# Kernel tuning notes

Hardware: AMD Instinct MI355X
Metric: run time of the kernel (lower is better)

## Reference

```python
import jax, jax.numpy as jnp
import numpy as np

E = 768      # embed_dim
H = 12       # num_heads
D = E // H   # head_dim = 64
G = 8        # num_groups (grouped 1x1 conv)
MAX_S = 197  # max_seq_len
RED = 8      # SE reduction ratio
S, B = 197, 64


def grouped_linear(x, w, b):
    """Grouped 1x1 conv as grouped linear. x: [..., Cin], w: [Cout, Cin//G], b: [Cout]."""
    cout = w.shape[0]
    cin = x.shape[-1]
    xg = x.reshape(x.shape[:-1] + (G, cin // G))
    wg = w.reshape(G, cout // G, cin // G)
    y = jnp.einsum('...gi,goi->...go', xg, wg)
    return y.reshape(x.shape[:-1] + (cout,)) + b


def channel_shuffle(x):
    """Shuffle channels (last dim) across G groups, matching torch channel_shuffle."""
    c = x.shape[-1]
    xg = x.reshape(x.shape[:-1] + (G, c // G))
    return jnp.swapaxes(xg, -1, -2).reshape(x.shape)


def layernorm(x, g, b, eps=1e-5):
    mu = jnp.mean(x, axis=-1, keepdims=True)
    var = jnp.var(x, axis=-1, keepdims=True)
    return (x - mu) * jax.lax.rsqrt(var + eps) * g + b


def setup_inputs() -> dict:
    rng = jax.random.key(0)
    ks = jax.random.split(rng, 16)
    std = 0.02
    return {
        'query': jax.random.normal(ks[0], (S, B, E), jnp.float32),
        'key':   jax.random.normal(ks[1], (S, B, E), jnp.float32),
        'value': jax.random.normal(ks[2], (S, B, E), jnp.float32),
        'qkv_w': jax.random.normal(ks[3], (3 * E, E // G), jnp.float32) * std,
        'qkv_b': jnp.zeros((3 * E,), jnp.float32),
        'out_w': jax.random.normal(ks[4], (E, E // G), jnp.float32) * std,
        'out_b': jnp.zeros((E,), jnp.float32),
        'rel_pos': jax.random.normal(ks[5], (2 * MAX_S - 1, D), jnp.float32) * std,
        'ln_g': jnp.ones((E,), jnp.float32),
        'ln_b': jnp.zeros((E,), jnp.float32),
        'fc1_w': jax.random.normal(ks[6], (E, E // RED), jnp.float32) * std,
        'fc1_b': jnp.zeros((E // RED,), jnp.float32),
        'fc2_w': jax.random.normal(ks[7], (E // RED, E), jnp.float32) * std,
        'fc2_b': jnp.zeros((E,), jnp.float32),
    }


def reference(query, key, value, qkv_w, qkv_b, out_w, out_b, rel_pos,
              ln_g, ln_b, fc1_w, fc1_b, fc2_w, fc2_b):
    seq_len, bsz, embed_dim = query.shape
    scaling = float(D) ** -0.5

    x = jnp.transpose(query, (1, 0, 2))              # [B, S, E]
    qkv = grouped_linear(x, qkv_w, qkv_b)            # [B, S, 3E]
    qkv = channel_shuffle(qkv)                       # [B, S, 3E]
    q, k, v = jnp.split(qkv, 3, axis=-1)             # each [B, S, E]

    def heads(t):                                    # [B, S, E] -> [B, H, S, D]
        return jnp.transpose(t.reshape(bsz, seq_len, H, D), (0, 2, 1, 3))
    q, k, v = heads(q) * scaling, heads(k), heads(v)

    attn_w = jnp.einsum('bhsd,bhtd->bhst', q, k)     # content-content

    # decoupled relative-position attention (note: slice, not skew, per source)
    rel = rel_pos[MAX_S - seq_len: MAX_S + seq_len - 1]           # [2S-1, D]
    content_pos = jnp.einsum('bhsd,rd->bhsr', q, rel)[..., seq_len - 1: 2 * seq_len - 1]
    pos_content = jnp.einsum('rd,bhtd->bhrt', rel, k)[:, :, seq_len - 1: 2 * seq_len - 1, :]
    attn_w = attn_w + content_pos + pos_content

    probs = jax.nn.softmax(attn_w, axis=-1)          # [B, H, S, S]
    attn = jnp.einsum('bhst,bhtd->bhsd', probs, v)   # [B, H, S, D]
    attn = jnp.transpose(attn, (0, 2, 1, 3)).reshape(bsz, seq_len, E)  # [B, S, E]

    # squeeze-excite style feature calibration gating
    scale = jax.nn.sigmoid(
        jnp.dot(jax.nn.gelu(jnp.dot(layernorm(attn, ln_g, ln_b), fc1_w) + fc1_b), fc2_w) + fc2_b)
    attn = attn * scale

    out = grouped_linear(attn, out_w, out_b)         # [B, S, E]
    out = jnp.transpose(out, (1, 0, 2))              # [S, B, E]

    avg_weights = jnp.sum(probs, axis=1) / H         # [B, S, S]
    return out, avg_weights
```

## Files before the change

kernel.cpp:

```cpp
#include <hip/hip_runtime.h>
#include <hip/hip_bf16.h>

constexpr int S = 197;
constexpr int B = 64;
constexpr int E = 768;
constexpr int H = 12;
constexpr int D = 64;
constexpr int M = S * B;
constexpr size_t SBE = (size_t)M * E;
constexpr int PST = 208;

typedef short bf16x8 __attribute__((ext_vector_type(8)));
typedef float f32x4 __attribute__((ext_vector_type(4)));
typedef unsigned int u32x4 __attribute__((ext_vector_type(4)));

__device__ __forceinline__ unsigned short f2b(float x) {
  unsigned int u = __float_as_uint(x);
  return (unsigned short)((u + 0x7FFFu + ((u >> 16) & 1u)) >> 16);
}
__device__ __forceinline__ float b2f(unsigned short u) {
  return __uint_as_float((unsigned int)u << 16);
}

__global__ __launch_bounds__(256) void mha_wprep(const float* __restrict__ w1,
                                                 const float* __restrict__ w2,
                                                 const float* __restrict__ lng,
                                                 const float* __restrict__ lnb,
                                                 const float* __restrict__ b1,
                                                 const float* __restrict__ rel,
                                                 unsigned short* __restrict__ w1t,
                                                 unsigned short* __restrict__ w2t,
                                                 float* __restrict__ cgb,
                                                 float* __restrict__ cbb,
                                                 unsigned short* __restrict__ relb) {
  const int bid = blockIdx.x, tid = threadIdx.x;
  if (bid < 288) {
    int idx = bid * 256 + tid;
    int n = idx / 768, k = idx - n * 768;
    w1t[idx] = f2b(lng[k] * w1[(size_t)k * 96 + n]);
  } else if (bid < 576) {
    int idx = (bid - 288) * 256 + tid;
    int n = idx / 96, k = idx - n * 96;
    w2t[idx] = f2b(w2[(size_t)k * 768 + n]);
  } else if (bid == 576) {
    if (tid < 96) {
      float cg = 0.f, cb = 0.f;
      for (int k = 0; k < 768; ++k) {
        float wv = w1[(size_t)k * 96 + tid];
        cg += lng[k] * wv;
        cb += lnb[k] * wv;
      }
      cgb[tid] = cg;
      cbb[tid] = cb + b1[tid];
    }
  } else {
    int idx = (bid - 577) * 256 + tid;
    int s2 = idx >> 6, d = idx & 63;
    float v = (s2 < S) ? rel[(size_t)(S - 1 + s2) * D + d] : 0.f;
    relb[idx] = f2b(v);
  }
}

__global__ __launch_bounds__(256) void mha_qkv_gemm(const float* __restrict__ x,
                                                    const float* __restrict__ w,
                                                    const float* __restrict__ bias,
                                                    unsigned short* __restrict__ y) {
  __shared__ __align__(16) unsigned short Xs[64 * 104];
  __shared__ __align__(16) unsigned short Wsl[96 * 104];
  __shared__ float bias_s[96];
  const int m0 = blockIdx.x * 64;
  const int n0 = blockIdx.y * 96;
  const int g = blockIdx.y / 3;
  const int tid = threadIdx.x;

  for (int i = tid; i < 64 * 24; i += 256) {
    int r = i / 24, c4 = i - r * 24;
    float4 v = *reinterpret_cast<const float4*>(
        &x[(size_t)(m0 + r) * E + g * 96 + c4 * 4]);
    unsigned short* dst = Xs + r * 104 + c4 * 4;
    dst[0] = f2b(v.x); dst[1] = f2b(v.y); dst[2] = f2b(v.z); dst[3] = f2b(v.w);
  }
  for (int i = tid; i < 96 * 24; i += 256) {
    int n = i / 24, c4 = i - n * 24;
    float4 v = *reinterpret_cast<const float4*>(&w[(size_t)(n0 + n) * 96 + c4 * 4]);
    unsigned short* dst = Wsl + n * 104 + c4 * 4;
    dst[0] = f2b(v.x); dst[1] = f2b(v.y); dst[2] = f2b(v.z); dst[3] = f2b(v.w);
  }
  if (tid < 96) bias_s[tid] = bias[n0 + tid];
  __syncthreads();

  const int lane = tid & 63, wv = tid >> 6;
  const int l15 = lane & 15, l4 = lane >> 4;

  const unsigned short* xrow = Xs + (16 * wv + l15) * 104 + l4 * 8;
  bf16x8 a0 = *(const bf16x8*)(xrow);
  bf16x8 a1 = *(const bf16x8*)(xrow + 32);
  bf16x8 a2 = *(const bf16x8*)(xrow + 64);

  f32x4 acc[6];
#pragma unroll
  for (int nf = 0; nf < 6; ++nf) acc[nf] = (f32x4){0.f, 0.f, 0.f, 0.f};
#pragma unroll
  for (int nf = 0; nf < 6; ++nf) {
    const unsigned short* wrow = Wsl + (nf * 16 + l15) * 104 + l4 * 8;
    f32x4 a = acc[nf];
    a = __builtin_amdgcn_mfma_f32_16x16x32_bf16(a0, *(const bf16x8*)(wrow), a, 0, 0, 0);
    a = __builtin_amdgcn_mfma_f32_16x16x32_bf16(a1, *(const bf16x8*)(wrow + 32), a, 0, 0, 0);
    a = __builtin_amdgcn_mfma_f32_16x16x32_bf16(a2, *(const bf16x8*)(wrow + 64), a, 0, 0, 0);
    acc[nf] = a;
  }

  const int mloc = m0 + 16 * wv + 4 * l4;
#pragma unroll
  for (int nf = 0; nf < 6; ++nf) {
    int p = nf * 16 + l15;
    float bv = bias_s[p];
#pragma unroll
    for (int r = 0; r < 4; ++r)
      y[(size_t)(mloc + r) * 2304 + n0 + p] = f2b(acc[nf][r] + bv);
  }
}

__global__ __launch_bounds__(256) void mha_qkv_shuffle(const unsigned short* __restrict__ y,
                                                       const float* __restrict__ rel,
                                                       unsigned short* __restrict__ qb,
                                                       unsigned short* __restrict__ kb,
                                                       unsigned short* __restrict__ vb) {
  const int tid = threadIdx.x;
  const int lane = tid & 63;
  const int g = lane >> 3, j = lane & 7;
  const int d = j * 8 + g;
  const int wrow = tid >> 6;
  const int rbase = blockIdx.x * 16;

  float relv[4];
  int sA[4], bA[4];
#pragma unroll
  for (int r8 = 0; r8 < 4; ++r8) {
    int rowl = rbase + r8 * 4 + wrow;
    sA[r8] = rowl >> 6;
    bA[r8] = rowl & 63;
    relv[r8] = rel[(size_t)(S - 1 + sA[r8]) * D + d];
  }

  for (int h = 0; h < H; ++h) {
#pragma unroll
    for (int r8 = 0; r8 < 4; ++r8) {
      int rowl = rbase + r8 * 4 + wrow;
      const unsigned short* yr = y + (size_t)rowl * 2304 + g * 288 + h * 8 + j;
      size_t o = (((size_t)bA[r8] * H + h) * S + sA[r8]) * D + d;
      float vq = b2f(yr[0]);
      float vk = b2f(yr[96]);
      float vv = b2f(yr[192]);
      qb[o] = f2b(0.125f * vq + relv[r8]);
      kb[o] = f2b(vk + relv[r8]);
      vb[o] = f2b(vv);
    }
  }
}

__global__ __launch_bounds__(256) void mha_fattn(
    const unsigned short* __restrict__ qb, const unsigned short* __restrict__ kb,
    const unsigned short* __restrict__ vb, const unsigned short* __restrict__ relb,
    float* __restrict__ context, unsigned short* __restrict__ probs, int bh0) {
  __shared__ __align__(16) unsigned short KtPt[64 * 136];
  __shared__ __align__(16) unsigned short Vh[64 * 136];
  unsigned short* Kt = KtPt;
  unsigned short* Pt = KtPt;

  const int id = blockIdx.x;
  const int xcd = id & 7;
  const int rr = id >> 3;
  const int stile = rr & 3;
  const int bhl = xcd + 8 * (rr >> 2);
  const int bh = bh0 + bhl;
  const int b_ = bh / H, h_ = bh - b_ * H;
  const int s0 = stile * 64;
  const int tid = threadIdx.x;
  const int lane = tid & 63, w = tid >> 6;
  const int l15 = lane & 15, l4 = lane >> 4;
  const int vt = tid & 63;
  const int vdb = (tid >> 6) * 8;

  const unsigned short* qg = qb + (((size_t)bh * S + (s0 + 16 * w + l15)) << 6) + l4 * 8;
  const unsigned short* rg = relb + (((size_t)(s0 + 16 * w + l15)) << 6) + l4 * 8;
  bf16x8 aq0 = *(const bf16x8*)(qg);
  bf16x8 aq1 = *(const bf16x8*)(qg + 32);
  bf16x8 aq2 = *(const bf16x8*)(rg);
  bf16x8 aq3 = *(const bf16x8*)(rg + 32);

  auto loadK = [&](int tc, u32x4* kv, u32x4* rv) {
#pragma unroll
    for (int ii = 0; ii < 2; ++ii) {
      int idx = tid + ii * 256;
      int r = idx >> 3, c = idx & 7;
      int tg = tc * 64 + r;
      kv[ii] = (u32x4){0, 0, 0, 0};
      rv[ii] = (u32x4){0, 0, 0, 0};
      if (tg < S) {
        kv[ii] = *(const u32x4*)(kb + (((size_t)bh * S + tg) << 6) + c * 8);
        u32x4 rvv = *(const u32x4*)(relb + ((size_t)tg << 6) + c * 8);
        rv[ii] = rvv ^ 0x80008000u;
      }
    }
  };

  f32x4 acc[13];
#pragma unroll
  for (int i = 0; i < 13; ++i) acc[i] = (f32x4){0.f, 0.f, 0.f, 0.f};

  u32x4 kvA[2], rvA[2], kvB[2], rvB[2];
  loadK(0, kvA, rvA);

#pragma unroll
  for (int tc = 0; tc < 4; ++tc) {
    u32x4* kvc = (tc & 1) ? kvB : kvA;
    u32x4* rvc = (tc & 1) ? rvB : rvA;
#pragma unroll
    for (int ii = 0; ii < 2; ++ii) {
      int idx = tid + ii * 256;
      int r = idx >> 3, c = idx & 7;
      *(u32x4*)(Kt + r * 136 + c * 8) = kvc[ii];
      *(u32x4*)(Kt + r * 136 + 64 + c * 8) = rvc[ii];
    }
    if (tc < 3) loadK(tc + 1, (tc & 1) ? kvA : kvB, (tc & 1) ? rvA : rvB);
    __syncthreads();
#pragma unroll
    for (int tf = 0; tf < 4; ++tf) {
      if (tc == 3 && tf > 0) continue;
      const unsigned short* kbse = Kt + (tf * 16 + l15) * 136 + l4 * 8;
      f32x4 a = acc[tc * 4 + tf];
      a = __builtin_amdgcn_mfma_f32_16x16x32_bf16(aq0, *(const bf16x8*)(kbse), a, 0, 0, 0);
      a = __builtin_amdgcn_mfma_f32_16x16x32_bf16(aq1, *(const bf16x8*)(kbse + 32), a, 0, 0, 0);
      a = __builtin_amdgcn_mfma_f32_16x16x32_bf16(aq2, *(const bf16x8*)(kbse + 64), a, 0, 0, 0);
      a = __builtin_amdgcn_mfma_f32_16x16x32_bf16(aq3, *(const bf16x8*)(kbse + 96), a, 0, 0, 0);
      acc[tc * 4 + tf] = a;
    }
    __syncthreads();
  }

  u32x4 v1[4];
#pragma unroll
  for (int ii = 0; ii < 4; ++ii) {
    int t = (ii & 1) * 64 + vt;
    int d0 = vdb + (ii >> 1) * 32;
    v1[ii] = *(const u32x4*)(vb + (((size_t)bh * S + t) << 6) + d0);
  }

  if (l15 >= 5) acc[12] = (f32x4){-3.0e38f, -3.0e38f, -3.0e38f, -3.0e38f};
  float inv[4];
#pragma unroll
  for (int r = 0; r < 4; ++r) {
    float m = acc[0][r];
#pragma unroll
    for (int tf = 1; tf < 13; ++tf) m = fmaxf(m, acc[tf][r]);
#pragma unroll
    for (int off = 1; off < 16; off <<= 1) m = fmaxf(m, __shfl_xor(m, off, 64));
    float s = 0.f;
#pragma unroll
    for (int tf = 0; tf < 13; ++tf) {
      float e = __expf(acc[tf][r] - m);
      acc[tf][r] = e;
      s += e;
    }
#pragma unroll
    for (int off = 1; off < 16; off <<= 1) s += __shfl_xor(s, off, 64);
    inv[r] = 1.f / s;
  }

  f32x4 ov[4];
#pragma unroll
  for (int df = 0; df < 4; ++df) ov[df] = (f32x4){0.f, 0.f, 0.f, 0.f};

#pragma unroll
  for (int tf = 0; tf < 8; ++tf)
#pragma unroll
    for (int r = 0; r < 4; ++r)
      Pt[(16 * w + 4 * l4 + r) * 136 + tf * 16 + l15] = f2b(acc[tf][r] * inv[r]);
#pragma unroll
  for (int ii = 0; ii < 4; ++ii) {
    int t = (ii & 1) * 64 + vt;
    int d0 = vdb + (ii >> 1) * 32;
    const unsigned short* vp = (const unsigned short*)&v1[ii];
#pragma unroll
    for (int j = 0; j < 8; ++j) Vh[(d0 + j) * 136 + t] = vp[j];
  }
  __syncthreads();

  u32x4 v2[4];
#pragma unroll
  for (int ii = 0; ii < 4; ++ii) {
    int t = 128 + (ii & 1) * 64 + vt;
    int d0 = vdb + (ii >> 1) * 32;
    v2[ii] = (u32x4){0, 0, 0, 0};
    if (t < S) v2[ii] = *(const u32x4*)(vb + (((size_t)bh * S + t) << 6) + d0);
  }

  {
    const int r2 = tid >> 2;
    const int sg = s0 + r2;
    if (sg < S) {
#pragma unroll
      for (int j = 0; j < 4; ++j) {
        int c = (tid & 3) + 4 * j;
        u32x4 pv = *(const u32x4*)(Pt + r2 * 136 + c * 8);
        *(u32x4*)(probs + ((size_t)bhl * S + sg) * PST + c * 8) = pv;
      }
    }
  }
  {
    bf16x8 ap[4];
#pragma unroll
    for (int kf = 0; kf < 4; ++kf)
      ap[kf] = *(const bf16x8*)(Pt + (16 * w + l15) * 136 + kf * 32 + l4 * 8);
#pragma unroll
    for (int df = 0; df < 4; ++df) {
      const unsigned short* vbse = Vh + (df * 16 + l15) * 136 + l4 * 8;
      f32x4 o = ov[df];
#pragma unroll
      for (int kf = 0; kf < 4; ++kf)
        o = __builtin_amdgcn_mfma_f32_16x16x32_bf16(ap[kf], *(const bf16x8*)(vbse + kf * 32), o, 0, 0, 0);
      ov[df] = o;
    }
  }
  __syncthreads();

#pragma unroll
  for (int tf = 8; tf < 13; ++tf)
#pragma unroll
    for (int r = 0; r < 4; ++r)
      Pt[(16 * w + 4 * l4 + r) * 136 + (tf - 8) * 16 + l15] = f2b(acc[tf][r] * inv[r]);
#pragma unroll
  for (int r = 0; r < 4; ++r)
    Pt[(16 * w + 4 * l4 + r) * 136 + 80 + l15] = 0;
#pragma unroll
  for (int ii = 0; ii < 4; ++ii) {
    int t0h = (ii & 1) * 64 + vt;
    int d0 = vdb + (ii >> 1) * 32;
    if (t0h < 96) {
      const unsigned short* vp = (const unsigned short*)&v2[ii];
#pragma unroll
      for (int j = 0; j < 8; ++j) Vh[(d0 + j) * 136 + t0h] = vp[j];
    }
  }
  __syncthreads();

  {
    const int r2 = tid >> 2;
    const int sg = s0 + r2;
    if (sg < S) {
#pragma unroll
      for (int j = 0; j < 3; ++j) {
        int c = (tid & 3) + 4 * j;
        if (c < 10) {
          u32x4 pv = *(const u32x4*)(Pt + r2 * 136 + c * 8);
          *(u32x4*)(probs + ((size_t)bhl * S + sg) * PST + 128 + c * 8) = pv;
        }
      }
    }
  }
  {
    bf16x8 ap[3];
#pragma unroll
    for (int kf = 0; kf < 3; ++kf)
      ap[kf] = *(const bf16x8*)(Pt + (16 * w + l15) * 136 + kf * 32 + l4 * 8);
#pragma unroll
    for (int df = 0; df < 4; ++df) {
      const unsigned short* vbse = Vh + (df * 16 + l15) * 136 + l4 * 8;
      f32x4 o = ov[df];
#pragma unroll
      for (int kf = 0; kf < 3; ++kf)
        o = __builtin_amdgcn_mfma_f32_16x16x32_bf16(ap[kf], *(const bf16x8*)(vbse + kf * 32), o, 0, 0, 0);
      ov[df] = o;
    }
  }

#pragma unroll
  for (int df = 0; df < 4; ++df)
#pragma unroll
    for (int r = 0; r < 4; ++r) {
      int sg = s0 + 16 * w + 4 * l4 + r;
      if (sg < S)
        context[((size_t)b_ * S + sg) * E + h_ * 64 + df * 16 + l15] = ov[df][r];
    }
}

__global__ __launch_bounds__(256) void mha_avgred(const unsigned short* __restrict__ probs,
                                                  float* __restrict__ avg, int b0) {
  const int bs = blockIdx.x;
  const int bl = bs / S, s = bs - bl * S;
  const int t = threadIdx.x;
  if (t >= S) return;
  float acc = 0.f;
#pragma unroll
  for (int h = 0; h < H; ++h)
    acc += b2f(probs[(((size_t)bl * H + h) * S + s) * PST + t]);
  avg[(((size_t)(b0 + bl)) * S + s) * S + t] = acc * (1.f / H);
}

__global__ __launch_bounds__(128) void mha_fc1ln(const float* __restrict__ ctx,
                                                 const unsigned short* __restrict__ w1t,
                                                 const float* __restrict__ cgb,
                                                 const float* __restrict__ cbb,
                                                 unsigned short* __restrict__ h1) {
  __shared__ __align__(16) unsigned short As[32 * 104];
  __shared__ __align__(16) unsigned short Wl[48 * 104];
  __shared__ float smu[32], sinv[32];
  const int m0 = blockIdx.x * 32;
  const int n0 = blockIdx.y * 48;
  const int tid = threadIdx.x;
  const int lane = tid & 63, w = tid >> 6;
  const int l15 = lane & 15, l4 = lane >> 4;
  const int r = tid >> 2, q = tid & 3;

  float s1 = 0.f, s2 = 0.f;
  f32x4 acc[3];
#pragma unroll
  for (int nf = 0; nf < 3; ++nf) acc[nf] = (f32x4){0.f, 0.f, 0.f, 0.f};

  for (int c = 0; c < 8; ++c) {
    const int k0 = c * 96;
    {
      const float* xr = ctx + (size_t)(m0 + r) * E + k0 + q * 24;
      unsigned short* ar = As + r * 104 + q * 24;
#pragma unroll
      for (int j = 0; j < 6; ++j) {
        float4 v = *reinterpret_cast<const float4*>(xr + j * 4);
        s1 += v.x + v.y + v.z + v.w;
        s2 += v.x * v.x + v.y * v.y + v.z * v.z + v.w * v.w;
        ar[j * 4 + 0] = f2b(v.x); ar[j * 4 + 1] = f2b(v.y);
        ar[j * 4 + 2] = f2b(v.z); ar[j * 4 + 3] = f2b(v.w);
      }
    }
    for (int i = tid; i < 48 * 12; i += 128) {
      int n = i / 12, c8 = i - n * 12;
      *(u32x4*)(Wl + n * 104 + c8 * 8) =
          *(const u32x4*)(w1t + (size_t)(n0 + n) * E + k0 + c8 * 8);
    }
    __syncthreads();
    const unsigned short* arow = As + (16 * w + l15) * 104 + l4 * 8;
    bf16x8 a0 = *(const bf16x8*)(arow);
    bf16x8 a1 = *(const bf16x8*)(arow + 32);
    bf16x8 a2 = *(const bf16x8*)(arow + 64);
#pragma unroll
    for (int nf = 0; nf < 3; ++nf) {
      const unsigned short* wr = Wl + (nf * 16 + l15) * 104 + l4 * 8;
      f32x4 a = acc[nf];
      a = __builtin_amdgcn_mfma_f32_16x16x32_bf16(a0, *(const bf16x8*)(wr), a, 0, 0, 0);
      a = __builtin_amdgcn_mfma_f32_16x16x32_bf16(a1, *(const bf16x8*)(wr + 32), a, 0, 0, 0);
      a = __builtin_amdgcn_mfma_f32_16x16x32_bf16(a2, *(const bf16x8*)(wr + 64), a, 0, 0, 0);
      acc[nf] = a;
    }
    __syncthreads();
  }

  s1 += __shfl_xor(s1, 1, 64); s1 += __shfl_xor(s1, 2, 64);
  s2 += __shfl_xor(s2, 1, 64); s2 += __shfl_xor(s2, 2, 64);
  if (q == 0) {
    float mu = s1 * (1.f / E);
    float var = s2 * (1.f / E) - mu * mu;
    smu[r] = mu;
    sinv[r] = rsqrtf(var + 1e-5f);
  }
  __syncthreads();

#pragma unroll
  for (int nf = 0; nf < 3; ++nf) {
    int n = n0 + nf * 16 + l15;
    float cg = cgb[n], cb = cbb[n];
#pragma unroll
    for (int rr = 0; rr < 4; ++rr) {
      int ml = 16 * w + 4 * l4 + rr;
      float u = sinv[ml] * (acc[nf][rr] - smu[ml] * cg) + cb;
      float gl = 0.5f * u * (1.f + tanhf(0.7978845608028654f * (u + 0.044715f * u * u * u)));
      h1[(size_t)(m0 + ml) * 96 + n] = f2b(gl);
    }
  }
}

__global__ __launch_bounds__(256) void mha_fc2(const unsigned short* __restrict__ h1,
                                               const unsigned short* __restrict__ w2t,
                                               const float* __restrict__ bias,
                                               const float* __restrict__ ctx,
                                               unsigned short* __restrict__ attn2) {
  __shared__ __align__(16) unsigned short Hs[64 * 104];
  __shared__ __align__(16) unsigned short Wl[192 * 104];
  const int m0 = blockIdx.x * 64;
  const int n0 = blockIdx.y * 192;
  const int tid = threadIdx.x;
  const int lane = tid & 63, w = tid >> 6;
  const int l15 = lane & 15, l4 = lane >> 4;

  for (int i = tid; i < 64 * 12; i += 256) {
    int rr = i / 12, c8 = i - rr * 12;
    *(u32x4*)(Hs + rr * 104 + c8 * 8) =
        *(const u32x4*)(h1 + (size_t)(m0 + rr) * 96 + c8 * 8);
  }
  for (int i = tid; i < 192 * 12; i += 256) {
    int n = i / 12, c8 = i - n * 12;
    *(u32x4*)(Wl + n * 104 + c8 * 8) =
        *(const u32x4*)(w2t + (size_t)(n0 + n) * 96 + c8 * 8);
  }
  __syncthreads();

  const unsigned short* arow = Hs + (16 * w + l15) * 104 + l4 * 8;
  bf16x8 a0 = *(const bf16x8*)(arow);
  bf16x8 a1 = *(const bf16x8*)(arow + 32);
  bf16x8 a2 = *(const bf16x8*)(arow + 64);

#pragma unroll
  for (int nf = 0; nf < 12; ++nf) {
    const unsigned short* wr = Wl + (nf * 16 + l15) * 104 + l4 * 8;
    f32x4 a = (f32x4){0.f, 0.f, 0.f, 0.f};
    a = __builtin_amdgcn_mfma_f32_16x16x32_bf16(a0, *(const bf16x8*)(wr), a, 0, 0, 0);
    a = __builtin_amdgcn_mfma_f32_16x16x32_bf16(a1, *(const bf16x8*)(wr + 32), a, 0, 0, 0);
    a = __builtin_amdgcn_mfma_f32_16x16x32_bf16(a2, *(const bf16x8*)(wr + 64), a, 0, 0, 0);
    int n = n0 + nf * 16 + l15;
    float bv = bias[n];
#pragma unroll
    for (int rr = 0; rr < 4; ++rr) {
      int m = m0 + 16 * w + 4 * l4 + rr;
      float val = a[rr] + bv;
      float sg = 1.f / (1.f + __expf(-val));
      float cv = ctx[(size_t)m * E + n];
      attn2[(size_t)m * E + n] = f2b(cv * sg);
    }
  }
}

__global__ __launch_bounds__(256) void mha_out(const unsigned short* __restrict__ attn2,
                                               const float* __restrict__ w,
                                               const float* __restrict__ bias,
                                               float* __restrict__ outp) {
  __shared__ __align__(16) unsigned short Asl[64 * 104];
  __shared__ __align__(16) unsigned short Wl[96 * 104];
  __shared__ float bias_s[96];
  const int m0 = blockIdx.x * 64;
  const int g = blockIdx.y;
  const int n0 = g * 96;
  const int tid = threadIdx.x;
  const int lane = tid & 63, w_ = tid >> 6;
  const int l15 = lane & 15, l4 = lane >> 4;

  for (int i = tid; i < 64 * 12; i += 256) {
    int rr = i / 12, c8 = i - rr * 12;
    *(u32x4*)(Asl + rr * 104 + c8 * 8) =
        *(const u32x4*)(attn2 + (size_t)(m0 + rr) * E + n0 + c8 * 8);
  }
  for (int i = tid; i < 96 * 24; i += 256) {
    int n = i / 24, c4 = i - n * 24;
    float4 v = *reinterpret_cast<const float4*>(&w[(size_t)(n0 + n) * 96 + c4 * 4]);
    unsigned short* dst = Wl + n * 104 + c4 * 4;
    dst[0] = f2b(v.x); dst[1] = f2b(v.y); dst[2] = f2b(v.z); dst[3] = f2b(v.w);
  }
  if (tid < 96) bias_s[tid] = bias[n0 + tid];
  __syncthreads();

  const unsigned short* arow = Asl + (16 * w_ + l15) * 104 + l4 * 8;
  bf16x8 a0 = *(const bf16x8*)(arow);
  bf16x8 a1 = *(const bf16x8*)(arow + 32);
  bf16x8 a2 = *(const bf16x8*)(arow + 64);

  int bb4[4], ss4[4];
#pragma unroll
  for (int rr = 0; rr < 4; ++rr) {
    int m = m0 + 16 * w_ + 4 * l4 + rr;
    bb4[rr] = m / S;
    ss4[rr] = m - bb4[rr] * S;
  }

#pragma unroll
  for (int nf = 0; nf < 6; ++nf) {
    const unsigned short* wr = Wl + (nf * 16 + l15) * 104 + l4 * 8;
    f32x4 a = (f32x4){0.f, 0.f, 0.f, 0.f};
    a = __builtin_amdgcn_mfma_f32_16x16x32_bf16(a0, *(const bf16x8*)(wr), a, 0, 0, 0);
    a = __builtin_amdgcn_mfma_f32_16x16x32_bf16(a1, *(const bf16x8*)(wr + 32), a, 0, 0, 0);
    a = __builtin_amdgcn_mfma_f32_16x16x32_bf16(a2, *(const bf16x8*)(wr + 64), a, 0, 0, 0);
    int p = n0 + nf * 16 + l15;
    float bv = bias_s[p - n0];
#pragma unroll
    for (int rr = 0; rr < 4; ++rr)
      outp[((size_t)ss4[rr] * B + bb4[rr]) * E + p] = a[rr] + bv;
  }
}

extern "C" void kernel_launch(void* const* d_in, const int* in_sizes, int n_in,
                              void* d_out, int out_size, void* d_ws, size_t ws_size,
                              hipStream_t stream) {
  const float* query = (const float*)d_in[0];
  const float* qkv_w = (const float*)d_in[3];
  const float* qkv_b = (const float*)d_in[4];
  const float* out_w = (const float*)d_in[5];
  const float* out_b = (const float*)d_in[6];
  const float* rel   = (const float*)d_in[7];
  const float* ln_g  = (const float*)d_in[8];
  const float* ln_b  = (const float*)d_in[9];
  const float* fc1_w = (const float*)d_in[10];
  const float* fc1_b = (const float*)d_in[11];
  const float* fc2_w = (const float*)d_in[12];
  const float* fc2_b = (const float*)d_in[13];

  float* ws = (float*)d_ws;
  unsigned short* qb   = (unsigned short*)ws;
  unsigned short* kbuf = qb + SBE;
  unsigned short* vbb  = kbuf + SBE;
  unsigned short* relb = vbb + SBE;
  size_t off = 3 * SBE / 2 + 8192;
  float* context = ws + off;
  unsigned short* attn2b = (unsigned short*)(ws + off + SBE);
  unsigned short* ybuf = (unsigned short*)context;
  unsigned short* h1b = attn2b + SBE;
  unsigned short* w1t = h1b + (size_t)M * 96;
  unsigned short* w2t = w1t + 73728;
  float* cgb = (float*)(w2t + 73728);
  float* cbb = cgb + 96;
  unsigned short* probsb = (unsigned short*)(cbb + 96);
  float* outp = (float*)d_out;
  float* avgp = outp + SBE;

  size_t used_f = off + SBE + (SBE + (size_t)M * 96 + 147456) / 2 + 192;
  size_t avail_f = (ws_size / 4 > used_f) ? ws_size / 4 - used_f : 0;
  int Bc = 2;
  const int cand[6] = {64, 32, 16, 8, 4, 2};
  for (int i = 0; i < 6; ++i) {
    size_t need_f = ((size_t)cand[i] * H * S * PST + 1) / 2;
    if (need_f <= avail_f) { Bc = cand[i]; break; }
  }

  mha_wprep<<<641, 256, 0, stream>>>(fc1_w, fc2_w, ln_g, ln_b, fc1_b, rel, w1t,
                                     w2t, cgb, cbb, relb);

  mha_qkv_gemm<<<dim3(M / 64, 24), 256, 0, stream>>>(query, qkv_w, qkv_b, ybuf);
  mha_qkv_shuffle<<<M / 16, 256, 0, stream>>>(ybuf, rel, qb, kbuf, vbb);

  for (int b0 = 0; b0 < B; b0 += Bc) {
    int bc = (B - b0 < Bc) ? (B - b0) : Bc;
    int nbh = bc * H;
    mha_fattn<<<4 * nbh, 256, 0, stream>>>(qb, kbuf, vbb, relb, context, probsb,
                                           b0 * H);
    mha_avgred<<<bc * S, 256, 0, stream>>>(probsb, avgp, b0);
  }

  mha_fc1ln<<<dim3(M / 32, 2), 128, 0, stream>>>(context, w1t, cgb, cbb, h1b);
  mha_fc2<<<dim3(M / 64, 4), 256, 0, stream>>>(h1b, w2t, fc2_b, context, attn2b);
  mha_out<<<dim3(M / 64, 8), 256, 0, stream>>>(attn2b, out_w, out_b, outp);
}
```

Measured before the change: 259.2 us.

## Pre-convert QKV input and weights to bf16 and drop LDS staging in QKV GEMM

A new elementwise kernel converts the fp32 query tensor to bf16 once, into a workspace slot (the q buffer) that is not written until after the GEMM. The weight-prep kernel gains extra blocks that convert the QKV weights to bf16. The QKV GEMM then loads MFMA fragments straight from global bf16 buffers, with no shared-memory staging or __syncthreads. This halves the bytes the GEMM reads and removes the repeated fp32-to-bf16 conversion, since each input column block is read by three N-tiles. The cost is an extra launch and an extra write and read of the bf16 copy of x.

```diff
diff --git a/kernel.cpp b/kernel.cpp
--- a/kernel.cpp
+++ b/kernel.cpp
@@ -28,11 +28,13 @@
                                                  const float* __restrict__ lnb,
                                                  const float* __restrict__ b1,
                                                  const float* __restrict__ rel,
+                                                 const float* __restrict__ wq,
                                                  unsigned short* __restrict__ w1t,
                                                  unsigned short* __restrict__ w2t,
                                                  float* __restrict__ cgb,
                                                  float* __restrict__ cbb,
-                                                 unsigned short* __restrict__ relb) {
+                                                 unsigned short* __restrict__ relb,
+                                                 unsigned short* __restrict__ wqt) {
   const int bid = blockIdx.x, tid = threadIdx.x;
   if (bid < 288) {
     int idx = bid * 256 + tid;
@@ -53,71 +55,56 @@
       cgb[tid] = cg;
       cbb[tid] = cb + b1[tid];
     }
-  } else {
+  } else if (bid < 641) {
     int idx = (bid - 577) * 256 + tid;
     int s2 = idx >> 6, d = idx & 63;
     float v = (s2 < S) ? rel[(size_t)(S - 1 + s2) * D + d] : 0.f;
     relb[idx] = f2b(v);
-  }
-}
-
-__global__ __launch_bounds__(256) void mha_qkv_gemm(const float* __restrict__ x,
-                                                    const float* __restrict__ w,
+  } else {
+    int idx = (bid - 641) * 256 + tid;
+    wqt[idx] = f2b(wq[idx]);
+  }
+}
+
+__global__ __launch_bounds__(256) void mha_xcvt(const float* __restrict__ x,
+                                                unsigned short* __restrict__ xb) {
+  size_t i = ((size_t)blockIdx.x * 256 + threadIdx.x) * 8;
+  float4 v0 = *reinterpret_cast<const float4*>(x + i);
+  float4 v1 = *reinterpret_cast<const float4*>(x + i + 4);
+  unsigned short o[8] = {f2b(v0.x), f2b(v0.y), f2b(v0.z), f2b(v0.w),
+                         f2b(v1.x), f2b(v1.y), f2b(v1.z), f2b(v1.w)};
+  *(u32x4*)(xb + i) = *(const u32x4*)o;
+}
+
+__global__ __launch_bounds__(256) void mha_qkv_gemm(const unsigned short* __restrict__ xb,
+                                                    const unsigned short* __restrict__ wqt,
                                                     const float* __restrict__ bias,
                                                     unsigned short* __restrict__ y) {
-  __shared__ __align__(16) unsigned short Xs[64 * 104];
-  __shared__ __align__(16) unsigned short Wsl[96 * 104];
-  __shared__ float bias_s[96];
   const int m0 = blockIdx.x * 64;
   const int n0 = blockIdx.y * 96;
   const int g = blockIdx.y / 3;
   const int tid = threadIdx.x;
-
-  for (int i = tid; i < 64 * 24; i += 256) {
-    int r = i / 24, c4 = i - r * 24;
-    float4 v = *reinterpret_cast<const float4*>(
-        &x[(size_t)(m0 + r) * E + g * 96 + c4 * 4]);
-    unsigned short* dst = Xs + r * 104 + c4 * 4;
-    dst[0] = f2b(v.x); dst[1] = f2b(v.y); dst[2] = f2b(v.z); dst[3] = f2b(v.w);
-  }
-  for (int i = tid; i < 96 * 24; i += 256) {
-    int n = i / 24, c4 = i - n * 24;
-    float4 v = *reinterpret_cast<const float4*>(&w[(size_t)(n0 + n) * 96 + c4 * 4]);
-    unsigned short* dst = Wsl + n * 104 + c4 * 4;
-    dst[0] = f2b(v.x); dst[1] = f2b(v.y); dst[2] = f2b(v.z); dst[3] = f2b(v.w);
-  }
-  if (tid < 96) bias_s[tid] = bias[n0 + tid];
-  __syncthreads();
-
   const int lane = tid & 63, wv = tid >> 6;
   const int l15 = lane & 15, l4 = lane >> 4;
 
-  const unsigned short* xrow = Xs + (16 * wv + l15) * 104 + l4 * 8;
-  bf16x8 a0 = *(const bf16x8*)(xrow);
-  bf16x8 a1 = *(const bf16x8*)(xrow + 32);
-  bf16x8 a2 = *(const bf16x8*)(xrow + 64);
-
-  f32x4 acc[6];
-#pragma unroll
-  for (int nf = 0; nf < 6; ++nf) acc[nf] = (f32x4){0.f, 0.f, 0.f, 0.f};
+  const unsigned short* xr = xb + (size_t)(m0 + 16 * wv + l15) * E + g * 96 + l4 * 8;
+  bf16x8 a0 = *(const bf16x8*)(xr);
+  bf16x8 a1 = *(const bf16x8*)(xr + 32);
+  bf16x8 a2 = *(const bf16x8*)(xr + 64);
+
+  const int mloc = m0 + 16 * wv + 4 * l4;
 #pragma unroll
   for (int nf = 0; nf < 6; ++nf) {
-    const unsigned short* wrow = Wsl + (nf * 16 + l15) * 104 + l4 * 8;
-    f32x4 a = acc[nf];
-    a = __builtin_amdgcn_mfma_f32_16x16x32_bf16(a0, *(const bf16x8*)(wrow), a, 0, 0, 0);
-    a = __builtin_amdgcn_mfma_f32_16x16x32_bf16(a1, *(const bf16x8*)(wrow + 32), a, 0, 0, 0);
-    a = __builtin_amdgcn_mfma_f32_16x16x32_bf16(a2, *(const bf16x8*)(wrow + 64), a, 0, 0, 0);
-    acc[nf] = a;
-  }
-
-  const int mloc = m0 + 16 * wv + 4 * l4;
-#pragma unroll
-  for (int nf = 0; nf < 6; ++nf) {
-    int p = nf * 16 + l15;
-    float bv = bias_s[p];
+    const unsigned short* wr = wqt + (size_t)(n0 + nf * 16 + l15) * 96 + l4 * 8;
+    f32x4 a = (f32x4){0.f, 0.f, 0.f, 0.f};
+    a = __builtin_amdgcn_mfma_f32_16x16x32_bf16(a0, *(const bf16x8*)(wr), a, 0, 0, 0);
+    a = __builtin_amdgcn_mfma_f32_16x16x32_bf16(a1, *(const bf16x8*)(wr + 32), a, 0, 0, 0);
+    a = __builtin_amdgcn_mfma_f32_16x16x32_bf16(a2, *(const bf16x8*)(wr + 64), a, 0, 0, 0);
+    int p = n0 + nf * 16 + l15;
+    float bv = bias[p];
 #pragma unroll
     for (int r = 0; r < 4; ++r)
-      y[(size_t)(mloc + r) * 2304 + n0 + p] = f2b(acc[nf][r] + bv);
+      y[(size_t)(mloc + r) * 2304 + p] = f2b(a[r] + bv);
   }
 }
 
@@ -602,6 +589,7 @@
 
   float* ws = (float*)d_ws;
   unsigned short* qb   = (unsigned short*)ws;
+  unsigned short* xbuf = qb;
   unsigned short* kbuf = qb + SBE;
   unsigned short* vbb  = kbuf + SBE;
   unsigned short* relb = vbb + SBE;
@@ -612,13 +600,14 @@
   unsigned short* h1b = attn2b + SBE;
   unsigned short* w1t = h1b + (size_t)M * 96;
   unsigned short* w2t = w1t + 73728;
-  float* cgb = (float*)(w2t + 73728);
+  unsigned short* wqt = w2t + 73728;
+  float* cgb = (float*)(wqt + 221184);
   float* cbb = cgb + 96;
   unsigned short* probsb = (unsigned short*)(cbb + 96);
   float* outp = (float*)d_out;
   float* avgp = outp + SBE;
 
-  size_t used_f = off + SBE + (SBE + (size_t)M * 96 + 147456) / 2 + 192;
+  size_t used_f = off + SBE + (SBE + (size_t)M * 96 + 368640) / 2 + 192;
   size_t avail_f = (ws_size / 4 > used_f) ? ws_size / 4 - used_f : 0;
   int Bc = 2;
   const int cand[6] = {64, 32, 16, 8, 4, 2};
@@ -627,10 +616,11 @@
     if (need_f <= avail_f) { Bc = cand[i]; break; }
   }
 
-  mha_wprep<<<641, 256, 0, stream>>>(fc1_w, fc2_w, ln_g, ln_b, fc1_b, rel, w1t,
-                                     w2t, cgb, cbb, relb);
-
-  mha_qkv_gemm<<<dim3(M / 64, 24), 256, 0, stream>>>(query, qkv_w, qkv_b, ybuf);
+  mha_wprep<<<1505, 256, 0, stream>>>(fc1_w, fc2_w, ln_g, ln_b, fc1_b, rel, qkv_w,
+                                      w1t, w2t, cgb, cbb, relb, wqt);
+  mha_xcvt<<<(int)(SBE / 8 / 256), 256, 0, stream>>>(query, xbuf);
+
+  mha_qkv_gemm<<<dim3(M / 64, 24), 256, 0, stream>>>(xbuf, wqt, qkv_b, ybuf);
   mha_qkv_shuffle<<<M / 16, 256, 0, stream>>>(ybuf, rel, qb, kbuf, vbb);
 
   for (int b0 = 0; b0 < B; b0 += Bc) {
```

Result: no change. 257.3 us (-0.7%).
